# Kernel optimization log

Hardware: AMD Instinct MI355X
Metric: run time of the kernel (lower is better)

The kernel has to match this reference:

```python
import jax, jax.numpy as jnp
import numpy as np

FEATURE_DIM = 1024
MAX_DEPTH = 32
HID = 128
N = 32768


def setup_inputs() -> dict:
    key = jax.random.key(0)
    ks = jax.random.split(key, 16)
    d = FEATURE_DIM
    s = 0.02
    return {
        "features": jax.random.normal(ks[0], (N, d), jnp.float32),
        "depths": jax.random.randint(ks[1], (N,), 0, MAX_DEPTH),
        "pos_emb": jax.random.normal(ks[2], (MAX_DEPTH, d), jnp.float32) * s,
        "aW1": jax.random.normal(ks[3], (HID, 2 * d), jnp.float32) * s,
        "ab1": jnp.zeros((HID,), jnp.float32),
        "aW2": jax.random.normal(ks[4], (1, HID), jnp.float32) * s,
        "ab2": jnp.zeros((1,), jnp.float32),
        "uW1": jax.random.normal(ks[5], (d, 2 * d), jnp.float32) * s,
        "ub1": jnp.zeros((d,), jnp.float32),
        "uW2": jax.random.normal(ks[6], (d, d), jnp.float32) * s,
        "ub2": jnp.zeros((d,), jnp.float32),
        "gW": jax.random.normal(ks[7], (d, 2 * d), jnp.float32) * s,
        "gb": jnp.zeros((d,), jnp.float32),
    }


def reference(features, depths, pos_emb, aW1, ab1, aW2, ab2,
              uW1, ub1, uW2, ub2, gW, gb):
    # add position embeddings (depths clamped to [0, MAX_DEPTH-1])
    dep = jnp.clip(depths, 0, MAX_DEPTH - 1)
    f = features + pos_emb[dep]                       # [N, d]
    target = f[0:1]                                    # [1, d]
    path = f[1:]                                       # [N-1, d]

    # attention MLP over all path states at once (vectorizes the torch loop)
    tb = jnp.broadcast_to(target, path.shape)          # [N-1, d]
    comb = jnp.concatenate([tb, path], axis=1)         # [N-1, 2d]
    h = jax.nn.relu(comb @ aW1.T + ab1)                # [N-1, 128]
    attn = jax.nn.sigmoid(h @ aW2.T + ab2)             # [N-1, 1]

    s = attn.sum()
    attn = jnp.where(s > 0, attn / s, attn)

    agg = (path * attn).sum(axis=0, keepdims=True)     # [1, d]
    c2 = jnp.concatenate([target, agg], axis=1)        # [1, 2d]
    gate = jax.nn.sigmoid(c2 @ gW.T + gb)
    upd = jax.nn.relu(c2 @ uW1.T + ub1) @ uW2.T + ub2
    updated_target = target + gate * upd
    return jnp.concatenate([updated_target, path], axis=0)
```

## Files before the change

### kernel.cpp

```cpp
#include <hip/hip_runtime.h>

#define DNUM 1024
#define HIDN 128
#define NTOT 32768
#define MR 32
#define NBLK 1024
#define NGRP 1024
#define TOTB (NGRP * 5)

#define T_OFF 0
#define P0_OFF 1024
#define S_OFF 1152
#define AGG_OFF 1216
#define GATE_OFF 2240
#define U1_OFF 3264
#define W2_FOFF 4288
#define AGGP_OFF (W2_FOFF + 65536)
#define SP_OFF (AGGP_OFF + NBLK * DNUM)
#define WS_NEED ((size_t)(SP_OFF + NBLK) * 4)

typedef __attribute__((ext_vector_type(8))) short short8;
typedef __attribute__((ext_vector_type(4))) float f32x4;

__device__ __forceinline__ unsigned short f2bf(float x) {
  unsigned int u = __builtin_bit_cast(unsigned int, x);
  u = u + 0x7fffu + ((u >> 16) & 1u);
  return (unsigned short)(u >> 16);
}
__device__ __forceinline__ float bf2f(unsigned int bits16) {
  unsigned int u = bits16 << 16;
  return __builtin_bit_cast(float, u);
}

__global__ __launch_bounds__(256) void kinit(const float* __restrict__ features,
                                             const int* __restrict__ depths,
                                             const float* __restrict__ pos_emb,
                                             const float* __restrict__ aW1,
                                             const float* __restrict__ ab1,
                                             float* __restrict__ ws,
                                             unsigned short* __restrict__ w2) {
  __shared__ float tgt[1024];
  __shared__ float ph[256];
  int t = threadIdx.x, bid = blockIdx.x;
  if (bid == 0) {
    int dep = depths[0];
    dep = dep < 0 ? 0 : (dep > 31 ? 31 : dep);
    float4 fv = *(const float4*)(features + t * 4);
    float4 pe = *(const float4*)(pos_emb + dep * DNUM + t * 4);
    float4 r;
    r.x = fv.x + pe.x; r.y = fv.y + pe.y; r.z = fv.z + pe.z; r.w = fv.w + pe.w;
    *(float4*)(ws + T_OFF + t * 4) = r;
    *(float4*)(tgt + t * 4) = r;
    float4 z = make_float4(0.f, 0.f, 0.f, 0.f);
    *(float4*)(ws + AGG_OFF + t * 4) = z;
    if (t < 64) ws[S_OFF + t] = 0.f;
    __syncthreads();
    int j = t >> 1, h = t & 1;
    const float* wrow = aW1 + (size_t)j * (2 * DNUM) + h * 512;
    const float* tr = tgt + h * 512;
    float p = 0.f;
    for (int k = 0; k < 512; k += 4) {
      float4 wv = *(const float4*)(wrow + k);
      float4 tv = *(const float4*)(tr + k);
      p += wv.x * tv.x + wv.y * tv.y + wv.z * tv.z + wv.w * tv.w;
    }
    ph[t] = p;
    __syncthreads();
    if (t < HIDN) ws[P0_OFF + t] = ab1[t] + ph[t * 2] + ph[t * 2 + 1];
    return;
  }
  int idx = ((bid - 1) * 256 + t) * 4;
  int j = idx >> 10, k = idx & 1023;
  float4 v = *(const float4*)(aW1 + (size_t)j * 2048 + 1024 + k);
  uint2 pk;
  pk.x = (unsigned int)f2bf(v.x) | ((unsigned int)f2bf(v.y) << 16);
  pk.y = (unsigned int)f2bf(v.z) | ((unsigned int)f2bf(v.w) << 16);
  *(uint2*)(w2 + idx) = pk;
}

__global__ __launch_bounds__(512) void kmain(
    const float* __restrict__ features, const int* __restrict__ depths,
    const float* __restrict__ pos_emb, const float* __restrict__ p0,
    const float* __restrict__ aW2, const float* __restrict__ ab2,
    const unsigned short* __restrict__ w2, float* __restrict__ out,
    float* __restrict__ agg, float* __restrict__ sacc,
    float* __restrict__ aggp, float* __restrict__ sp) {
  __shared__ __align__(16) unsigned char ldsA[MR * 2048];
  __shared__ float part[160];
  __shared__ float comb[1024];
  const int t = threadIdx.x;
  const int b = blockIdx.x;
  const int q = b / 5;
  const int r5 = b - q * 5;
  const int tc = t & 255;
  const int th = t >> 8;
  const int col = tc * 4;

  if (r5 != 0) {
    const int s = q * 4 + (r5 - 1);
#pragma unroll
    for (int iter = 0; iter < 4; ++iter) {
      int i = iter * 2 + th;
      int fr = 1 + s * 8 + i;
      if (fr < NTOT) {
        int dp = depths[fr];
        dp = dp < 0 ? 0 : (dp > 31 ? 31 : dp);
        float4 fv = *(const float4*)(features + (size_t)fr * DNUM + col);
        float4 pe = *(const float4*)(pos_emb + (size_t)dp * DNUM + col);
        float4 f;
        f.x = fv.x + pe.x; f.y = fv.y + pe.y; f.z = fv.z + pe.z; f.w = fv.w + pe.w;
        *(float4*)(out + (size_t)fr * DNUM + col) = f;
      }
    }
    return;
  }

  const int bid = q;
  const int lane = t & 63;
  const int w = t >> 6;
  const int llo = lane & 15;
  const int lhi = lane >> 4;

#pragma unroll
  for (int ii = 0; ii < 16; ++ii) {
    int i = ii * 2 + th;
    int fr = 1 + bid * MR + i;
    float4 f = make_float4(0.f, 0.f, 0.f, 0.f);
    if (fr < NTOT) {
      int dp = depths[fr];
      dp = dp < 0 ? 0 : (dp > 31 ? 31 : dp);
      float4 fv = *(const float4*)(features + (size_t)fr * DNUM + col);
      float4 pe = *(const float4*)(pos_emb + (size_t)dp * DNUM + col);
      f.x = fv.x + pe.x; f.y = fv.y + pe.y; f.z = fv.z + pe.z; f.w = fv.w + pe.w;
    }
    uint2 pk;
    pk.x = (unsigned int)f2bf(f.x) | ((unsigned int)f2bf(f.y) << 16);
    pk.y = (unsigned int)f2bf(f.z) | ((unsigned int)f2bf(f.w) << 16);
    int off = (i * 2048 + tc * 8) ^ ((i & 7) << 4);
    *(uint2*)(ldsA + off) = pk;
  }
  __syncthreads();

  const int wm = w >> 2, wn = w & 3;
  f32x4 acc[2];
  acc[0] = (f32x4){0.f, 0.f, 0.f, 0.f};
  acc[1] = (f32x4){0.f, 0.f, 0.f, 0.f};
  const int arow = wm * 16 + llo;
  const int abase = arow * 2048;
  const int aswz = (arow & 7) << 4;
  const unsigned short* bpA = w2 + (size_t)(wn * 32 + llo) * DNUM + lhi * 8;
  const unsigned short* bpB = bpA + 16 * DNUM;

#pragma unroll 4
  for (int kc = 0; kc < 32; ++kc) {
    int kbase = kc * 32;
    short8 av = *(short8*)(ldsA + ((abase + (kbase + lhi * 8) * 2) ^ aswz));
    short8 bv0 = *(const short8*)(bpA + kbase);
    short8 bv1 = *(const short8*)(bpB + kbase);
    acc[0] = __builtin_amdgcn_mfma_f32_16x16x32_bf16(av, bv0, acc[0], 0, 0, 0);
    acc[1] = __builtin_amdgcn_mfma_f32_16x16x32_bf16(av, bv1, acc[1], 0, 0, 0);
  }

  float p0v[2], wv[2];
#pragma unroll
  for (int n = 0; n < 2; ++n) {
    int j = wn * 32 + n * 16 + llo;
    p0v[n] = p0[j];
    wv[n] = aW2[j];
  }
#pragma unroll
  for (int e = 0; e < 4; ++e) {
    float s = 0.f;
#pragma unroll
    for (int n = 0; n < 2; ++n) {
      float h = acc[n][e] + p0v[n];
      h = fmaxf(h, 0.f);
      s += h * wv[n];
    }
    s += __shfl_xor(s, 1);
    s += __shfl_xor(s, 2);
    s += __shfl_xor(s, 4);
    s += __shfl_xor(s, 8);
    if (llo == 0) part[wn * 32 + wm * 16 + lhi * 4 + e] = s;
  }
  __syncthreads();

  if (t < MR) {
    float pre = part[t] + part[32 + t] + part[64 + t] + part[96 + t] + ab2[0];
    int fr = 1 + bid * MR + t;
    float raw = 0.f;
    if (fr < NTOT) raw = 1.f / (1.f + __expf(-pre));
    part[128 + t] = raw;
  }
  __syncthreads();

  float a0 = 0.f, a1 = 0.f, a2 = 0.f, a3 = 0.f;
  for (int lr = th * 16; lr < th * 16 + 16; ++lr) {
    float r = part[128 + lr];
    int off = (lr * 2048 + tc * 8) ^ ((lr & 7) << 4);
    uint2 pk = *(uint2*)(ldsA + off);
    a0 += r * bf2f(pk.x & 0xffffu);
    a1 += r * bf2f(pk.x >> 16);
    a2 += r * bf2f(pk.y & 0xffffu);
    a3 += r * bf2f(pk.y >> 16);
  }
  if (th == 1) {
    comb[tc * 4 + 0] = a0; comb[tc * 4 + 1] = a1;
    comb[tc * 4 + 2] = a2; comb[tc * 4 + 3] = a3;
  }
  __syncthreads();
  if (th == 0) {
    float c0 = a0 + comb[tc * 4 + 0];
    float c1 = a1 + comb[tc * 4 + 1];
    float c2v = a2 + comb[tc * 4 + 2];
    float c3 = a3 + comb[tc * 4 + 3];
    if (aggp) {
      f32x4 v = {c0, c1, c2v, c3};
      *(f32x4*)(aggp + (size_t)bid * DNUM + col) = v;
    } else {
      atomicAdd(agg + col + 0, c0);
      atomicAdd(agg + col + 1, c1);
      atomicAdd(agg + col + 2, c2v);
      atomicAdd(agg + col + 3, c3);
    }
  }
  if (t == 0) {
    float s = 0.f;
    for (int lr = 0; lr < MR; ++lr) s += part[128 + lr];
    if (sp) sp[bid] = s;
    else atomicAdd(sacc + (bid & 63), s);
  }
}

__global__ __launch_bounds__(256) void kred(const float* __restrict__ aggp,
                                            const float* __restrict__ sp,
                                            float* __restrict__ ws) {
  int t = threadIdx.x, bid = blockIdx.x;
  if (bid < 256) {
    int w = t >> 6, lane = t & 63;
    int colIdx = bid * 4 + w;
    float s = 0.f;
#pragma unroll 4
    for (int k = 0; k < NBLK / 64; ++k) {
      int r = lane + k * 64;
      s += aggp[(size_t)r * DNUM + colIdx];
    }
    s += __shfl_xor(s, 1);
    s += __shfl_xor(s, 2);
    s += __shfl_xor(s, 4);
    s += __shfl_xor(s, 8);
    s += __shfl_xor(s, 16);
    s += __shfl_xor(s, 32);
    if (lane == 0) ws[AGG_OFF + colIdx] = s;
  } else {
    __shared__ float red[256];
    float s = 0.f;
    for (int k = t; k < NBLK; k += 256) s += sp[k];
    red[t] = s;
    __syncthreads();
    if (t < 64) {
      float v = red[t] + red[t + 64] + red[t + 128] + red[t + 192];
      v += __shfl_xor(v, 1);
      v += __shfl_xor(v, 2);
      v += __shfl_xor(v, 4);
      v += __shfl_xor(v, 8);
      v += __shfl_xor(v, 16);
      v += __shfl_xor(v, 32);
      if (t == 0) ws[S_OFF] = v;
    }
  }
}

__global__ __launch_bounds__(256) void kc1(const float* __restrict__ gW,
                                           const float* __restrict__ gb,
                                           const float* __restrict__ uW1,
                                           const float* __restrict__ ub1,
                                           float* __restrict__ ws) {
  __shared__ float c2[2048];
  __shared__ float sinv_sh;
  int t = threadIdx.x, bid = blockIdx.x;
  if (t == 0) {
    float s = 0.f;
    for (int i = 0; i < 64; ++i) s += ws[S_OFF + i];
    sinv_sh = (s > 0.f) ? 1.f / s : 1.f;
  }
  __syncthreads();
  float sinv = sinv_sh;
  for (int i = t; i < 2048; i += 256)
    c2[i] = (i < 1024) ? ws[T_OFF + i] : ws[AGG_OFF + i - 1024] * sinv;
  __syncthreads();
  int w = t >> 6, lane = t & 63;
  int isGate = bid < 256;
  int o = (isGate ? bid : bid - 256) * 4 + w;
  const float* W = isGate ? gW : uW1;
  float p = 0.f;
  for (int i = lane; i < 2048; i += 64) p += W[(size_t)o * 2048 + i] * c2[i];
  p += __shfl_xor(p, 1);
  p += __shfl_xor(p, 2);
  p += __shfl_xor(p, 4);
  p += __shfl_xor(p, 8);
  p += __shfl_xor(p, 16);
  p += __shfl_xor(p, 32);
  if (lane == 0) {
    float v = p + (isGate ? gb[o] : ub1[o]);
    v = isGate ? (1.f / (1.f + expf(-v))) : fmaxf(v, 0.f);
    ws[(isGate ? GATE_OFF : U1_OFF) + o] = v;
  }
}

__global__ __launch_bounds__(256) void kc2(const float* __restrict__ uW2,
                                           const float* __restrict__ ub2,
                                           const float* __restrict__ ws,
                                           float* __restrict__ out) {
  __shared__ float u1[1024];
  int t = threadIdx.x, bid = blockIdx.x;
  for (int i = t; i < 1024; i += 256) u1[i] = ws[U1_OFF + i];
  __syncthreads();
  int w = t >> 6, lane = t & 63;
  int o = bid * 4 + w;
  float p = 0.f;
  for (int i = lane; i < 1024; i += 64) p += uW2[(size_t)o * 1024 + i] * u1[i];
  p += __shfl_xor(p, 1);
  p += __shfl_xor(p, 2);
  p += __shfl_xor(p, 4);
  p += __shfl_xor(p, 8);
  p += __shfl_xor(p, 16);
  p += __shfl_xor(p, 32);
  if (lane == 0) {
    float upd = p + ub2[o];
    out[o] = ws[T_OFF + o] + ws[GATE_OFF + o] * upd;
  }
}

extern "C" void kernel_launch(void* const* d_in, const int* in_sizes, int n_in,
                              void* d_out, int out_size, void* d_ws, size_t ws_size,
                              hipStream_t stream) {
  const float* features = (const float*)d_in[0];
  const int* depths = (const int*)d_in[1];
  const float* pos_emb = (const float*)d_in[2];
  const float* aW1 = (const float*)d_in[3];
  const float* ab1 = (const float*)d_in[4];
  const float* aW2 = (const float*)d_in[5];
  const float* ab2 = (const float*)d_in[6];
  const float* uW1 = (const float*)d_in[7];
  const float* ub1 = (const float*)d_in[8];
  const float* uW2 = (const float*)d_in[9];
  const float* ub2 = (const float*)d_in[10];
  const float* gW = (const float*)d_in[11];
  const float* gb = (const float*)d_in[12];
  float* out = (float*)d_out;
  float* ws = (float*)d_ws;
  unsigned short* w2 = (unsigned short*)(ws + W2_FOFF);
  bool useP = ws_size >= WS_NEED;
  float* aggp = useP ? (ws + AGGP_OFF) : nullptr;
  float* sp = useP ? (ws + SP_OFF) : nullptr;

  hipLaunchKernelGGL(kinit, dim3(129), dim3(256), 0, stream,
                     features, depths, pos_emb, aW1, ab1, ws, w2);
  hipLaunchKernelGGL(kmain, dim3(TOTB), dim3(512), 0, stream,
                     features, depths, pos_emb, ws + P0_OFF, aW2, ab2, w2, out,
                     ws + AGG_OFF, ws + S_OFF, aggp, sp);
  if (useP)
    hipLaunchKernelGGL(kred, dim3(257), dim3(256), 0, stream, aggp, sp, ws);
  hipLaunchKernelGGL(kc1, dim3(512), dim3(256), 0, stream, gW, gb, uW1, ub1, ws);
  hipLaunchKernelGGL(kc2, dim3(256), dim3(256), 0, stream, uW2, ub2, ws, out);
}
```

Baseline: 190.2 us.

## Drop LDS staging; load MFMA A operands directly from global and reload for aggregation

The 64KB LDS tile of bf16 path rows is removed. Each MFMA lane now loads its features and pos_emb slices straight from global memory, adds them, and packs to bf16 with v_cvt_pk_bf16_f32. The aggregation pass re-reads the rows in fp32 from global, which also removes the bf16 rounding in agg. Launch bounds now request higher occupancy. The aim is to trade LDS capacity and the staging barrier for more resident blocks, at the cost of extra global/L2 traffic from reading each row twice with less coalesced per-lane accesses.

```diff
diff --git a/kernel.cpp b/kernel.cpp
--- a/kernel.cpp
+++ b/kernel.cpp
@@ -5,8 +5,7 @@
 #define NTOT 32768
 #define MR 32
 #define NBLK 1024
-#define NGRP 1024
-#define TOTB (NGRP * 5)
+#define TOTB (NBLK * 5)
 
 #define T_OFF 0
 #define P0_OFF 1024
@@ -21,15 +20,17 @@
 
 typedef __attribute__((ext_vector_type(8))) short short8;
 typedef __attribute__((ext_vector_type(4))) float f32x4;
+typedef __attribute__((ext_vector_type(4))) unsigned int u32x4;
 
 __device__ __forceinline__ unsigned short f2bf(float x) {
   unsigned int u = __builtin_bit_cast(unsigned int, x);
   u = u + 0x7fffu + ((u >> 16) & 1u);
   return (unsigned short)(u >> 16);
 }
-__device__ __forceinline__ float bf2f(unsigned int bits16) {
-  unsigned int u = bits16 << 16;
-  return __builtin_bit_cast(float, u);
+__device__ __forceinline__ unsigned int cvtpk(float lo, float hi) {
+  unsigned int r;
+  asm("v_cvt_pk_bf16_f32 %0, %1, %2" : "=v"(r) : "v"(lo), "v"(hi));
+  return r;
 }
 
 __global__ __launch_bounds__(256) void kinit(const float* __restrict__ features,
@@ -78,16 +79,16 @@
   *(uint2*)(w2 + idx) = pk;
 }
 
-__global__ __launch_bounds__(512) void kmain(
+__global__ __launch_bounds__(512, 4) void kmain(
     const float* __restrict__ features, const int* __restrict__ depths,
     const float* __restrict__ pos_emb, const float* __restrict__ p0,
     const float* __restrict__ aW2, const float* __restrict__ ab2,
     const unsigned short* __restrict__ w2, float* __restrict__ out,
     float* __restrict__ agg, float* __restrict__ sacc,
     float* __restrict__ aggp, float* __restrict__ sp) {
-  __shared__ __align__(16) unsigned char ldsA[MR * 2048];
   __shared__ float part[160];
   __shared__ float comb[1024];
+  __shared__ int depsL[MR];
   const int t = threadIdx.x;
   const int b = blockIdx.x;
   const int q = b / 5;
@@ -100,8 +101,7 @@
     const int s = q * 4 + (r5 - 1);
 #pragma unroll
     for (int iter = 0; iter < 4; ++iter) {
-      int i = iter * 2 + th;
-      int fr = 1 + s * 8 + i;
+      int fr = 1 + s * 8 + iter * 2 + th;
       if (fr < NTOT) {
         int dp = depths[fr];
         dp = dp < 0 ? 0 : (dp > 31 ? 31 : dp);
@@ -120,43 +120,44 @@
   const int w = t >> 6;
   const int llo = lane & 15;
   const int lhi = lane >> 4;
-
-#pragma unroll
-  for (int ii = 0; ii < 16; ++ii) {
-    int i = ii * 2 + th;
-    int fr = 1 + bid * MR + i;
-    float4 f = make_float4(0.f, 0.f, 0.f, 0.f);
-    if (fr < NTOT) {
-      int dp = depths[fr];
-      dp = dp < 0 ? 0 : (dp > 31 ? 31 : dp);
-      float4 fv = *(const float4*)(features + (size_t)fr * DNUM + col);
-      float4 pe = *(const float4*)(pos_emb + (size_t)dp * DNUM + col);
-      f.x = fv.x + pe.x; f.y = fv.y + pe.y; f.z = fv.z + pe.z; f.w = fv.w + pe.w;
-    }
-    uint2 pk;
-    pk.x = (unsigned int)f2bf(f.x) | ((unsigned int)f2bf(f.y) << 16);
-    pk.y = (unsigned int)f2bf(f.z) | ((unsigned int)f2bf(f.w) << 16);
-    int off = (i * 2048 + tc * 8) ^ ((i & 7) << 4);
-    *(uint2*)(ldsA + off) = pk;
-  }
-  __syncthreads();
-
   const int wm = w >> 2, wn = w & 3;
+
+  if (t < MR) {
+    int fr = 1 + bid * MR + t;
+    int dp = (fr < NTOT) ? depths[fr] : 0;
+    dp = dp < 0 ? 0 : (dp > 31 ? 31 : dp);
+    depsL[t] = dp;
+  }
+
+  const int arow = wm * 16 + llo;
+  int fr_a = 1 + bid * MR + arow;
+  if (fr_a > NTOT - 1) fr_a = NTOT - 1;
+  int dpa = depths[fr_a];
+  dpa = dpa < 0 ? 0 : (dpa > 31 ? 31 : dpa);
+  const float* frow = features + (size_t)fr_a * DNUM + lhi * 8;
+  const float* prow = pos_emb + (size_t)dpa * DNUM + lhi * 8;
+  const unsigned short* bpA = w2 + (size_t)(wn * 32 + llo) * DNUM + lhi * 8;
+  const unsigned short* bpB = bpA + 16 * DNUM;
+
   f32x4 acc[2];
   acc[0] = (f32x4){0.f, 0.f, 0.f, 0.f};
   acc[1] = (f32x4){0.f, 0.f, 0.f, 0.f};
-  const int arow = wm * 16 + llo;
-  const int abase = arow * 2048;
-  const int aswz = (arow & 7) << 4;
-  const unsigned short* bpA = w2 + (size_t)(wn * 32 + llo) * DNUM + lhi * 8;
-  const unsigned short* bpB = bpA + 16 * DNUM;
 
 #pragma unroll 4
   for (int kc = 0; kc < 32; ++kc) {
-    int kbase = kc * 32;
-    short8 av = *(short8*)(ldsA + ((abase + (kbase + lhi * 8) * 2) ^ aswz));
-    short8 bv0 = *(const short8*)(bpA + kbase);
-    short8 bv1 = *(const short8*)(bpB + kbase);
+    int kb = kc * 32;
+    f32x4 fa = *(const f32x4*)(frow + kb);
+    f32x4 fb = *(const f32x4*)(frow + kb + 4);
+    f32x4 pa = *(const f32x4*)(prow + kb);
+    f32x4 pb = *(const f32x4*)(prow + kb + 4);
+    u32x4 pk;
+    pk.x = cvtpk(fa.x + pa.x, fa.y + pa.y);
+    pk.y = cvtpk(fa.z + pa.z, fa.w + pa.w);
+    pk.z = cvtpk(fb.x + pb.x, fb.y + pb.y);
+    pk.w = cvtpk(fb.z + pb.z, fb.w + pb.w);
+    short8 av = __builtin_bit_cast(short8, pk);
+    short8 bv0 = *(const short8*)(bpA + kb);
+    short8 bv1 = *(const short8*)(bpB + kb);
     acc[0] = __builtin_amdgcn_mfma_f32_16x16x32_bf16(av, bv0, acc[0], 0, 0, 0);
     acc[1] = __builtin_amdgcn_mfma_f32_16x16x32_bf16(av, bv1, acc[1], 0, 0, 0);
   }
@@ -196,13 +197,15 @@
 
   float a0 = 0.f, a1 = 0.f, a2 = 0.f, a3 = 0.f;
   for (int lr = th * 16; lr < th * 16 + 16; ++lr) {
+    int fr = 1 + bid * MR + lr;
+    if (fr >= NTOT) break;
     float r = part[128 + lr];
-    int off = (lr * 2048 + tc * 8) ^ ((lr & 7) << 4);
-    uint2 pk = *(uint2*)(ldsA + off);
-    a0 += r * bf2f(pk.x & 0xffffu);
-    a1 += r * bf2f(pk.x >> 16);
-    a2 += r * bf2f(pk.y & 0xffffu);
-    a3 += r * bf2f(pk.y >> 16);
+    float4 fv = *(const float4*)(features + (size_t)fr * DNUM + col);
+    float4 pe = *(const float4*)(pos_emb + (size_t)depsL[lr] * DNUM + col);
+    a0 += r * (fv.x + pe.x);
+    a1 += r * (fv.y + pe.y);
+    a2 += r * (fv.z + pe.z);
+    a3 += r * (fv.w + pe.w);
   }
   if (th == 1) {
     comb[tc * 4 + 0] = a0; comb[tc * 4 + 1] = a1;
```

Result: slower. 347.2 us (+82.5%).
